# Kernel optimization log

Measured on AMD Instinct MI355X. Metric: run time of the kernel, lower is better.

## Reference

```python
import jax, jax.numpy as jnp
import numpy as np

B, T, C = 2, 2048, 1024
H = 4 * C           # MLP hidden (4*n_embd)
E_DYN = 7           # num_experts - static_experts
TOP_K = 2           # num_experts_per_tok
MOE_LOSS_COEF = 0.01


def setup_inputs() -> dict:
    key = jax.random.key(0)
    ks = jax.random.split(key, 6)
    s = 0.02
    x = jax.random.normal(ks[0], (B, T, C), dtype=jnp.float32)
    gate_w = jax.random.normal(ks[1], (C, E_DYN), dtype=jnp.float32) * s
    w1 = jax.random.normal(ks[2], (E_DYN, C, H), dtype=jnp.float32) * s   # dynamic experts c_fc
    w2 = jax.random.normal(ks[3], (E_DYN, H, C), dtype=jnp.float32) * s   # dynamic experts c_proj
    w1s = jax.random.normal(ks[4], (C, H), dtype=jnp.float32) * s         # static expert c_fc
    w2s = jax.random.normal(ks[5], (H, C), dtype=jnp.float32) * s         # static expert c_proj
    return {"x": x, "gate_w": gate_w, "w1": w1, "w2": w2, "w1s": w1s, "w2s": w2s}


def reference(x, gate_w, w1, w2, w1s, w2s):
    b, t, c = x.shape
    xf = x.reshape(-1, c)                                   # [N, C]
    n = xf.shape[0]

    # static expert (always applied)
    y_static = jax.nn.gelu(xf @ w1s, approximate=False) @ w2s  # [N, C]

    # gating: top-k + softmax over selected scores
    scores = xf @ gate_w                                    # [N, E]
    topk_scores, topk_idx = jax.lax.top_k(scores, TOP_K)    # [N, K]
    topk_w = jax.nn.softmax(topk_scores, axis=-1)           # [N, K]

    # dense dispatch weights [N, E] (top_k indices are distinct -> set is safe)
    probs = jnp.zeros((n, E_DYN), dtype=x.dtype)
    probs = probs.at[jnp.arange(n)[:, None], topk_idx].set(topk_w)

    # all-expert MLP then weighted combine (same math as masked per-expert dispatch)
    h = jax.nn.gelu(jnp.einsum('nc,ech->enh', xf, w1), approximate=False)  # [E, N, H]
    y_all = jnp.einsum('enh,ehc->enc', h, w2)               # [E, N, C]
    y_dyn = jnp.einsum('ne,enc->nc', probs, y_all)          # [N, C]

    y = (y_dyn + y_static).reshape(b, t, c)

    # variance_penalty auxiliary loss
    expert_usage = probs.mean(axis=0)                       # [E]
    variance = jnp.mean((expert_usage - expert_usage.mean()) ** 2)
    aux = MOE_LOSS_COEF * variance
    return y, aux
```

## Files before the change

kernel.cpp:

```cpp
#include <hip/hip_runtime.h>
#include <hip/hip_bf16.h>
#include <math.h>

#define N_TOK 4096
#define C_DIM 1024
#define H_DIM 4096
#define NEXP 7
#define NGRP 8
#define HCAP 13184

typedef __attribute__((ext_vector_type(8))) short short8;
typedef __attribute__((ext_vector_type(4))) float floatx4;

static const size_t OFF_COUNTS = 0;
static const size_t OFF_CURSOR = 64;
static const size_t OFF_BASE   = 128;
static const size_t OFF_PCOUNT = 192;
static const size_t OFF_CNT8   = 256;
static const size_t OFF_USAGE  = 320;
static const size_t OFF_TOPKI  = 4096;
static const size_t OFF_TOPKW  = OFF_TOPKI + 8192ull * 4;
static const size_t OFF_ETOK   = OFF_TOPKW + 8192ull * 4;
static const size_t OFF_EWT    = OFF_ETOK + (size_t)HCAP * 4;
static const size_t OFF_EIDX   = OFF_EWT + (size_t)HCAP * 4;
static const size_t OFF_XB     = 262144;
static const size_t OFF_W1T    = OFF_XB + (size_t)N_TOK * C_DIM * 2;
static const size_t OFF_W2T    = OFF_W1T + (size_t)NGRP * H_DIM * C_DIM * 2;
static const size_t OFF_H      = OFF_W2T + (size_t)NGRP * C_DIM * H_DIM * 2;

static __device__ __forceinline__ unsigned short f2bf(float f) {
    __hip_bfloat16 b = __float2bfloat16(f);
    return *reinterpret_cast<unsigned short*>(&b);
}
static __device__ __forceinline__ float bf2f(unsigned short u) {
    unsigned int v = ((unsigned int)u) << 16;
    return __builtin_bit_cast(float, v);
}

static __device__ __forceinline__ float gelu_f(float v) {
    float z = v * 0.70710678118654752f;
    float az = fabsf(z);
    float t = 1.0f / (1.0f + 0.3275911f * az);
    float poly = t * (0.254829592f + t * (-0.284496736f + t * (1.421413741f +
                 t * (-1.453152027f + t * 1.061405429f))));
    float erf_abs = 1.0f - poly * __expf(-az * az);
    float erf_v = (z < 0.f) ? -erf_abs : erf_abs;
    return 0.5f * v * (1.0f + erf_v);
}

static __device__ __forceinline__ void gll16(const void* g, void* l) {
    __builtin_amdgcn_global_load_lds((const __attribute__((address_space(1))) void*)g,
                                     (__attribute__((address_space(3))) void*)l, 16, 0, 0);
}

static __device__ __forceinline__ void barf() {
    __builtin_amdgcn_s_barrier();
    asm volatile("" ::: "memory");
}
static __device__ __forceinline__ void lgkm0s() {
    asm volatile("s_waitcnt lgkmcnt(0)" ::: "memory");
    __builtin_amdgcn_sched_barrier(0);
}

__global__ void init_small_kernel(int* counts, int* cursor, float* usage) {
    int i = threadIdx.x;
    if (i < 8) { counts[i] = 0; cursor[i] = 0; usage[i] = 0.f; }
}

__global__ __launch_bounds__(256) void transpose_cvt_kernel(
    const float* __restrict__ dyn, const float* __restrict__ stat,
    __hip_bfloat16* __restrict__ dst, int R, int S)
{
    int e = blockIdx.z;
    const float* src = (e < NEXP) ? (dyn + (size_t)e * R * S) : stat;
    unsigned short* d = (unsigned short*)(dst + (size_t)e * R * S);
    int s0 = blockIdx.x * 64, r0 = blockIdx.y * 64;
    __shared__ float t[64][65];
    int lx = (threadIdx.x & 15) * 4, ty = threadIdx.x >> 4;
#pragma unroll
    for (int i = 0; i < 4; i++) {
        int r = ty + i * 16;
        float4 v = *(const float4*)(src + (size_t)(r0 + r) * S + s0 + lx);
        t[r][lx] = v.x; t[r][lx + 1] = v.y; t[r][lx + 2] = v.z; t[r][lx + 3] = v.w;
    }
    __syncthreads();
#pragma unroll
    for (int i = 0; i < 4; i++) {
        int ss = ty + i * 16;
        ushort4 o;
        o.x = f2bf(t[lx][ss]); o.y = f2bf(t[lx + 1][ss]);
        o.z = f2bf(t[lx + 2][ss]); o.w = f2bf(t[lx + 3][ss]);
        *(ushort4*)(d + (size_t)(s0 + ss) * R + r0 + lx) = o;
    }
}

__global__ __launch_bounds__(256) void gate_kernel(
    const float* __restrict__ x, const float* __restrict__ gw,
    unsigned short* __restrict__ xb,
    int* __restrict__ topki, float* __restrict__ topkw,
    int* counts, float* usage)
{
    int wid = threadIdx.x >> 6, lane = threadIdx.x & 63;
    int t = blockIdx.x * 4 + wid;
    float s[NEXP];
#pragma unroll
    for (int e = 0; e < NEXP; e++) s[e] = 0.f;
#pragma unroll
    for (int it = 0; it < 4; ++it) {
        int c = it * 256 + lane * 4;
        float4 xv = *(const float4*)(x + (size_t)t * C_DIM + c);
        ushort4 o;
        o.x = f2bf(xv.x); o.y = f2bf(xv.y); o.z = f2bf(xv.z); o.w = f2bf(xv.w);
        *(ushort4*)(xb + (size_t)t * C_DIM + c) = o;
        const float* g0 = gw + (size_t)c * NEXP;
#pragma unroll
        for (int e = 0; e < NEXP; e++) s[e] += xv.x * g0[e];
#pragma unroll
        for (int e = 0; e < NEXP; e++) s[e] += xv.y * g0[NEXP + e];
#pragma unroll
        for (int e = 0; e < NEXP; e++) s[e] += xv.z * g0[2 * NEXP + e];
#pragma unroll
        for (int e = 0; e < NEXP; e++) s[e] += xv.w * g0[3 * NEXP + e];
    }
#pragma unroll
    for (int e = 0; e < NEXP; e++)
        for (int off = 32; off > 0; off >>= 1) s[e] += __shfl_xor(s[e], off);
    if (lane == 0) {
        int e0 = 0;
        for (int e = 1; e < NEXP; e++) if (s[e] > s[e0]) e0 = e;
        int e1 = -1;
        for (int e = 0; e < NEXP; e++) {
            if (e == e0) continue;
            if (e1 < 0 || s[e] > s[e1]) e1 = e;
        }
        float w0 = 1.f / (1.f + expf(s[e1] - s[e0]));
        float w1 = 1.f - w0;
        topki[t * 2] = e0; topki[t * 2 + 1] = e1;
        topkw[t * 2] = w0; topkw[t * 2 + 1] = w1;
        atomicAdd(&counts[e0], 1); atomicAdd(&counts[e1], 1);
        atomicAdd(&usage[e0], w0); atomicAdd(&usage[e1], w1);
    }
}

__global__ __launch_bounds__(256) void prefix_kernel(
    const int* counts, const float* usage,
    int* base, int* pcount, int* cnt8,
    int* etok, float* ewt, float* y, int aux_index)
{
    __shared__ int sb[NGRP], sc[NGRP], sp[NGRP];
    if (threadIdx.x == 0) {
        int run = 0;
        for (int g = 0; g < NEXP; g++) {
            int c = counts[g];
            int p = (c + 127) & ~127;
            base[g] = run; pcount[g] = p; cnt8[g] = c;
            sb[g] = run; sc[g] = c; sp[g] = p;
            run += p;
        }
        base[NEXP] = run; pcount[NEXP] = N_TOK; cnt8[NEXP] = N_TOK;
        sb[NEXP] = run; sc[NEXP] = N_TOK; sp[NEXP] = N_TOK;
        float u[NEXP]; float mean = 0.f;
        for (int e = 0; e < NEXP; e++) { u[e] = usage[e] / (float)N_TOK; mean += u[e]; }
        mean /= (float)NEXP;
        float var = 0.f;
        for (int e = 0; e < NEXP; e++) { float dd = u[e] - mean; var += dd * dd; }
        var /= (float)NEXP;
        y[aux_index] = 0.01f * var;
    }
    __syncthreads();
    for (int i = threadIdx.x; i < N_TOK; i += 256) {
        etok[sb[NEXP] + i] = i; ewt[sb[NEXP] + i] = 1.0f;
    }
    for (int g = 0; g < NEXP; g++) {
        for (int i = sc[g] + (int)threadIdx.x; i < sp[g]; i += 256) {
            etok[sb[g] + i] = 0; ewt[sb[g] + i] = 0.f;
        }
    }
}

__global__ void scatter_kernel(const int* __restrict__ topki, const float* __restrict__ topkw,
                               const int* __restrict__ base, int* cursor,
                               int* __restrict__ etok, float* __restrict__ ewt,
                               int* __restrict__ eidx)
{
    int i = blockIdx.x * 256 + threadIdx.x;
    int t = i >> 1;
    int e = topki[i];
    float w = topkw[i];
    int pos = atomicAdd(&cursor[e], 1);
    int idx = base[e] + pos;
    etok[idx] = t; ewt[idx] = w;
    eidx[i] = idx;
}


static __device__ __forceinline__ void mfma16(const short8 (&a)[8], const short8 (&b)[4],
                                              floatx4 (&acc)[8][4], int mo, int no) {
#pragma unroll
    for (int i = 0; i < 4; i++)
#pragma unroll
        for (int j = 0; j < 2; j++)
#pragma unroll
            for (int kk = 0; kk < 2; kk++)
                acc[mo + i][no + j] = __builtin_amdgcn_mfma_f32_16x16x32_bf16(
                    a[i * 2 + kk], b[j * 2 + kk], acc[mo + i][no + j], 0, 0, 0);
}
static __device__ __forceinline__ void rdA(short8 (&d)[8], const char* b, int sw0, int sw1) {
#pragma unroll
    for (int i = 0; i < 4; i++) {
        d[i * 2]     = *(const short8*)(b + i * 2048 + sw0);
        d[i * 2 + 1] = *(const short8*)(b + i * 2048 + sw1);
    }
}
static __device__ __forceinline__ void rdB(short8 (&d)[4], const char* b, int sw0, int sw1) {
#pragma unroll
    for (int j = 0; j < 2; j++) {
        d[j * 2]     = *(const short8*)(b + j * 2048 + sw0);
        d[j * 2 + 1] = *(const short8*)(b + j * 2048 + sw1);
    }
}

static __device__ __forceinline__ void gemm_core(char* lds, int NKT,
    const char* pA0, const char* pA1, const char* pA2, const char* pA3,
    const char* pB0, const char* pB1, const char* pB2, const char* pB3,
    floatx4 (&acc)[8][4])
{
    int tid = threadIdx.x, lane = tid & 63, w = tid >> 6;
    int wm = w >> 2, wn = w & 3, l16 = lane & 15, quad = lane >> 4;
    int sw0 = ((quad ^ (l16 & 7)) << 4);
    int sw1 = (((4 + quad) ^ (l16 & 7)) << 4);
    int aoff = (wm * 64 + l16) * 128;
    int boff = (wn * 32 + l16) * 128;
    int wb = w * 1024;
    short8 aM0[8], aM1[8], bN0[4], bN1[4];

#define SA_(h, doff, ko) do { \
    gll16(((h) ? pA1 : pA0) + (ko), lds + (doff) + (h) * 16384 + wb); \
    gll16(((h) ? pA3 : pA2) + (ko), lds + (doff) + (h) * 16384 + 8192 + wb); } while (0)
#define SB_(nh, doff, ko) do { \
    gll16(((nh) ? pB1 : pB0) + (ko), lds + 65536 + (doff) + (nh) * 16384 + wb); \
    gll16(((nh) ? pB3 : pB2) + (ko), lds + 65536 + (doff) + (nh) * 16384 + 8192 + wb); } while (0)

    SA_(0, 0, 0); SA_(1, 0, 0); SB_(0, 0, 0); SB_(1, 0, 0);
    SA_(0, 32768, 128); SA_(1, 32768, 128); SB_(0, 32768, 128);
    asm volatile("s_waitcnt vmcnt(6)" ::: "memory");
    barf();

#pragma unroll 1
    for (int T = 0; T < NKT; ++T) {
        int curo = (T & 1) << 15;
        int nxto = curo ^ 32768;
        bool st1 = (T + 1 < NKT), st2 = (T + 2 < NKT);
        rdA(aM0, lds + curo + aoff, sw0, sw1);
        rdB(bN0, lds + 65536 + curo + boff, sw0, sw1);
        if (st1) SB_(1, nxto, 128);
        barf(); lgkm0s();
        __builtin_amdgcn_s_setprio(1); mfma16(aM0, bN0, acc, 0, 0); __builtin_amdgcn_s_setprio(0);
        barf();
        rdA(aM1, lds + curo + 16384 + aoff, sw0, sw1);
        if (st2) SA_(0, curo, 256);
        barf(); lgkm0s();
        __builtin_amdgcn_s_setprio(1); mfma16(aM1, bN0, acc, 4, 0); __builtin_amdgcn_s_setprio(0);
        barf();
        rdB(bN1, lds + 65536 + curo + 16384 + boff, sw0, sw1);
        if (st2) SA_(1, curo, 256);
        barf(); lgkm0s();
        __builtin_amdgcn_s_setprio(1); mfma16(aM0, bN1, acc, 0, 2); __builtin_amdgcn_s_setprio(0);
        barf();
        if (st2) SB_(0, curo, 256);
        barf();
        __builtin_amdgcn_s_setprio(1); mfma16(aM1, bN1, acc, 4, 2); __builtin_amdgcn_s_setprio(0);
        if (T >= NKT - 2) { asm volatile("s_waitcnt vmcnt(0)" ::: "memory"); }
        else              { asm volatile("s_waitcnt vmcnt(6)" ::: "memory"); }
        barf();
        pA0 += 128; pA1 += 128; pA2 += 128; pA3 += 128;
        pB0 += 128; pB1 += 128; pB2 += 128; pB3 += 128;
    }
#undef SA_
#undef SB_
}

__global__ __launch_bounds__(512, 2) void gemm1_kernel(
    const __hip_bfloat16* __restrict__ xb,
    const __hip_bfloat16* __restrict__ w1t,
    __hip_bfloat16* __restrict__ h,
    const int* __restrict__ etok,
    const int* __restrict__ base,
    const int* __restrict__ pcount)
{
    int id = blockIdx.x;
    int xcd = id & 7, rest = id >> 3;
    int ct = rest & 15, s = rest >> 4;
    int g = s & 7;
    int mt = ((xcd - g) & 7) + 8 * (s >> 3);
    int psz = pcount[g];
    if (mt * 256 >= psz) return;
    int eb = base[g];

    __shared__ __align__(16) char lds[131072];

    int tid = threadIdx.x, lane = tid & 63, w = tid >> 6;
    int u0 = 8 * w + (lane >> 3);
    int v  = (u0 & 31) + ((u0 >> 5) << 6);
    int ssw = ((lane & 7) ^ (lane >> 3)) * 16;

    int t0 = etok[eb + mt * 256 + u0];
    int t1 = etok[eb + mt * 256 + 64 + u0];
    int t2 = etok[eb + mt * 256 + 128 + u0];
    int t3 = etok[eb + mt * 256 + 192 + u0];
    const char* pA0 = (const char*)(xb + (size_t)t0 * C_DIM) + ssw;
    const char* pA1 = (const char*)(xb + (size_t)t1 * C_DIM) + ssw;
    const char* pA2 = (const char*)(xb + (size_t)t2 * C_DIM) + ssw;
    const char* pA3 = (const char*)(xb + (size_t)t3 * C_DIM) + ssw;
    const char* pB0 = (const char*)(w1t + ((size_t)g * H_DIM + ct * 256 + v) * C_DIM) + ssw;
    const char* pB1 = (const char*)(w1t + ((size_t)g * H_DIM + ct * 256 + v + 32) * C_DIM) + ssw;
    const char* pB2 = (const char*)(w1t + ((size_t)g * H_DIM + ct * 256 + v + 128) * C_DIM) + ssw;
    const char* pB3 = (const char*)(w1t + ((size_t)g * H_DIM + ct * 256 + v + 160) * C_DIM) + ssw;

    floatx4 acc[8][4] = {};
    gemm_core(lds, C_DIM / 64, pA0, pA1, pA2, pA3, pB0, pB1, pB2, pB3, acc);

    int wm = w >> 2, wn = w & 3, l16 = lane & 15, quad = lane >> 4;
#pragma unroll
    for (int i = 0; i < 8; i++) {
        int lr0 = mt * 256 + wm * 128 + i * 16 + quad * 4;
#pragma unroll
        for (int reg = 0; reg < 4; reg++) {
            int lr = lr0 + reg;
            if (lr < psz) {
                size_t hrow = (size_t)(eb + lr) * H_DIM;
#pragma unroll
                for (int j = 0; j < 4; j++) {
                    int cc = ct * 256 + wn * 64 + j * 16 + l16;
                    h[hrow + cc] = __float2bfloat16(gelu_f(acc[i][j][reg]));
                }
            }
        }
    }
}

__global__ __launch_bounds__(512, 2) void gemm2_kernel(
    const __hip_bfloat16* __restrict__ h,
    const __hip_bfloat16* __restrict__ w2t,
    unsigned short* __restrict__ yp,
    const int* __restrict__ base,
    const int* __restrict__ pcount)
{
    int id = blockIdx.x;
    int xcd = id & 7, rest = id >> 3;
    int ct = rest & 3, s = rest >> 2;
    int g = s & 7;
    int mt = ((xcd - g) & 7) + 8 * (s >> 3);
    int psz = pcount[g];
    if (mt * 256 >= psz) return;
    int eb = base[g];

    __shared__ __align__(16) char lds[131072];

    int tid = threadIdx.x, lane = tid & 63, w = tid >> 6;
    int u0 = 8 * w + (lane >> 3);
    int v  = (u0 & 31) + ((u0 >> 5) << 6);
    int ssw = ((lane & 7) ^ (lane >> 3)) * 16;

    const char* pA0 = (const char*)(h + (size_t)(eb + mt * 256 + u0) * H_DIM) + ssw;
    const char* pA1 = (const char*)(h + (size_t)(eb + mt * 256 + 64 + u0) * H_DIM) + ssw;
    const char* pA2 = (const char*)(h + (size_t)(eb + mt * 256 + 128 + u0) * H_DIM) + ssw;
    const char* pA3 = (const char*)(h + (size_t)(eb + mt * 256 + 192 + u0) * H_DIM) + ssw;
    const char* pB0 = (const char*)(w2t + ((size_t)g * C_DIM + ct * 256 + v) * H_DIM) + ssw;
    const char* pB1 = (const char*)(w2t + ((size_t)g * C_DIM + ct * 256 + v + 32) * H_DIM) + ssw;
    const char* pB2 = (const char*)(w2t + ((size_t)g * C_DIM + ct * 256 + v + 128) * H_DIM) + ssw;
    const char* pB3 = (const char*)(w2t + ((size_t)g * C_DIM + ct * 256 + v + 160) * H_DIM) + ssw;

    floatx4 acc[8][4] = {};
    gemm_core(lds, H_DIM / 64, pA0, pA1, pA2, pA3, pB0, pB1, pB2, pB3, acc);

    int wm = w >> 2, wn = w & 3, l16 = lane & 15, quad = lane >> 4;
#pragma unroll
    for (int i = 0; i < 8; i++) {
        int lr0 = mt * 256 + wm * 128 + i * 16 + quad * 4;
#pragma unroll
        for (int reg = 0; reg < 4; reg++) {
            int lr = lr0 + reg;
            if (lr < psz) {
                size_t yrow = (size_t)(eb + lr) * C_DIM;
#pragma unroll
                for (int j = 0; j < 4; j++) {
                    int cc = ct * 256 + wn * 64 + j * 16 + l16;
                    yp[yrow + cc] = f2bf(acc[i][j][reg]);
                }
            }
        }
    }
}

__global__ __launch_bounds__(256) void combine_kernel(
    const unsigned short* __restrict__ yp,
    const int* __restrict__ eidx,
    const float* __restrict__ topkw,
    const int* __restrict__ base,
    float* __restrict__ y)
{
    int t = blockIdx.x;
    int i0 = eidx[t * 2], i1 = eidx[t * 2 + 1];
    float w0 = topkw[t * 2], w1 = topkw[t * 2 + 1];
    int is = base[NEXP] + t;
    int c = threadIdx.x * 4;
    ushort4 a = *(const ushort4*)(yp + (size_t)i0 * C_DIM + c);
    ushort4 b = *(const ushort4*)(yp + (size_t)i1 * C_DIM + c);
    ushort4 s = *(const ushort4*)(yp + (size_t)is * C_DIM + c);
    float4 o;
    o.x = w0 * bf2f(a.x) + w1 * bf2f(b.x) + bf2f(s.x);
    o.y = w0 * bf2f(a.y) + w1 * bf2f(b.y) + bf2f(s.y);
    o.z = w0 * bf2f(a.z) + w1 * bf2f(b.z) + bf2f(s.z);
    o.w = w0 * bf2f(a.w) + w1 * bf2f(b.w) + bf2f(s.w);
    *(float4*)(y + (size_t)t * C_DIM + c) = o;
}

extern "C" void kernel_launch(void* const* d_in, const int* in_sizes, int n_in,
                              void* d_out, int out_size, void* d_ws, size_t ws_size,
                              hipStream_t stream) {
    const float* x      = (const float*)d_in[0];
    const float* gate_w = (const float*)d_in[1];
    const float* w1     = (const float*)d_in[2];
    const float* w2     = (const float*)d_in[3];
    const float* w1s    = (const float*)d_in[4];
    const float* w2s    = (const float*)d_in[5];
    float* y = (float*)d_out;
    char* ws = (char*)d_ws;

    int*   counts = (int*)(ws + OFF_COUNTS);
    int*   cursor = (int*)(ws + OFF_CURSOR);
    int*   base   = (int*)(ws + OFF_BASE);
    int*   pcount = (int*)(ws + OFF_PCOUNT);
    int*   cnt8   = (int*)(ws + OFF_CNT8);
    float* usage  = (float*)(ws + OFF_USAGE);
    int*   topki  = (int*)(ws + OFF_TOPKI);
    float* topkw  = (float*)(ws + OFF_TOPKW);
    int*   etok   = (int*)(ws + OFF_ETOK);
    float* ewt    = (float*)(ws + OFF_EWT);
    int*   eidx   = (int*)(ws + OFF_EIDX);
    unsigned short* xb_u = (unsigned short*)(ws + OFF_XB);
    __hip_bfloat16* xb  = (__hip_bfloat16*)(ws + OFF_XB);
    __hip_bfloat16* w1t = (__hip_bfloat16*)(ws + OFF_W1T);
    __hip_bfloat16* w2t = (__hip_bfloat16*)(ws + OFF_W2T);
    __hip_bfloat16* hbuf = (__hip_bfloat16*)(ws + OFF_H);
    unsigned short* yp  = (unsigned short*)(ws + OFF_W1T);

    init_small_kernel<<<1, 64, 0, stream>>>(counts, cursor, usage);

    transpose_cvt_kernel<<<dim3(H_DIM / 64, C_DIM / 64, NGRP), 256, 0, stream>>>(w1, w1s, w1t, C_DIM, H_DIM);
    transpose_cvt_kernel<<<dim3(C_DIM / 64, H_DIM / 64, NGRP), 256, 0, stream>>>(w2, w2s, w2t, H_DIM, C_DIM);

    gate_kernel<<<N_TOK / 4, 256, 0, stream>>>(x, gate_w, xb_u, topki, topkw, counts, usage);
    prefix_kernel<<<1, 256, 0, stream>>>(counts, usage, base, pcount, cnt8, etok, ewt, y, N_TOK * C_DIM);
    scatter_kernel<<<(N_TOK * 2) / 256, 256, 0, stream>>>(topki, topkw, base, cursor, etok, ewt, eidx);

    gemm1_kernel<<<4096, 512, 0, stream>>>(xb, w1t, hbuf, etok, base, pcount);
    gemm2_kernel<<<1024, 512, 0, stream>>>(hbuf, w2t, yp, base, pcount);
    combine_kernel<<<N_TOK, 256, 0, stream>>>(yp, eidx, topkw, base, y);
}
```

Baseline: 726.7 us.

## Peel GEMM mainloop tail and merge weight transpose launches into one

```diff
diff --git a/kernel.cpp b/kernel.cpp
--- a/kernel.cpp
+++ b/kernel.cpp
@@ -57,10 +57,11 @@
     __builtin_amdgcn_s_barrier();
     asm volatile("" ::: "memory");
 }
-static __device__ __forceinline__ void lgkm0s() {
-    asm volatile("s_waitcnt lgkmcnt(0)" ::: "memory");
-    __builtin_amdgcn_sched_barrier(0);
-}
+#define LGKM0 asm volatile("s_waitcnt lgkmcnt(0)" ::: "memory")
+#define VMC6  asm volatile("s_waitcnt vmcnt(6)" ::: "memory")
+#define VMC0  asm volatile("s_waitcnt vmcnt(0)" ::: "memory")
+#define PRIO1 __builtin_amdgcn_s_setprio(1)
+#define PRIO0 __builtin_amdgcn_s_setprio(0)
 
 __global__ void init_small_kernel(int* counts, int* cursor, float* usage) {
     int i = threadIdx.x;
@@ -68,20 +69,35 @@
 }
 
 __global__ __launch_bounds__(256) void transpose_cvt_kernel(
-    const float* __restrict__ dyn, const float* __restrict__ stat,
-    __hip_bfloat16* __restrict__ dst, int R, int S)
-{
-    int e = blockIdx.z;
-    const float* src = (e < NEXP) ? (dyn + (size_t)e * R * S) : stat;
-    unsigned short* d = (unsigned short*)(dst + (size_t)e * R * S);
-    int s0 = blockIdx.x * 64, r0 = blockIdx.y * 64;
+    const float* __restrict__ w1, const float* __restrict__ w1s,
+    const float* __restrict__ w2, const float* __restrict__ w2s,
+    __hip_bfloat16* __restrict__ w1t, __hip_bfloat16* __restrict__ w2t)
+{
+    int bid = blockIdx.x;
+    int fam = bid >> 13;
+    int r = bid & 8191;
+    int e = r >> 10;
+    int t_ = r & 1023;
+    int R, S, s0, r0;
+    const float* src; unsigned short* d;
+    if (fam == 0) {
+        R = C_DIM; S = H_DIM;
+        src = (e < NEXP) ? (w1 + (size_t)e * R * S) : w1s;
+        d = (unsigned short*)(w1t) + (size_t)e * R * S;
+        s0 = (t_ & 63) * 64; r0 = (t_ >> 6) * 64;
+    } else {
+        R = H_DIM; S = C_DIM;
+        src = (e < NEXP) ? (w2 + (size_t)e * R * S) : w2s;
+        d = (unsigned short*)(w2t) + (size_t)e * R * S;
+        s0 = (t_ & 15) * 64; r0 = (t_ >> 4) * 64;
+    }
     __shared__ float t[64][65];
     int lx = (threadIdx.x & 15) * 4, ty = threadIdx.x >> 4;
 #pragma unroll
     for (int i = 0; i < 4; i++) {
-        int r = ty + i * 16;
-        float4 v = *(const float4*)(src + (size_t)(r0 + r) * S + s0 + lx);
-        t[r][lx] = v.x; t[r][lx + 1] = v.y; t[r][lx + 2] = v.z; t[r][lx + 3] = v.w;
+        int rr = ty + i * 16;
+        float4 v = *(const float4*)(src + (size_t)(r0 + rr) * S + s0 + lx);
+        t[rr][lx] = v.x; t[rr][lx + 1] = v.y; t[rr][lx + 2] = v.z; t[rr][lx + 3] = v.w;
     }
     __syncthreads();
 #pragma unroll
@@ -243,38 +259,66 @@
 
     SA_(0, 0, 0); SA_(1, 0, 0); SB_(0, 0, 0); SB_(1, 0, 0);
     SA_(0, 32768, 128); SA_(1, 32768, 128); SB_(0, 32768, 128);
-    asm volatile("s_waitcnt vmcnt(6)" ::: "memory");
+    VMC6;
     barf();
 
 #pragma unroll 1
-    for (int T = 0; T < NKT; ++T) {
+    for (int T = 0; T < NKT - 2; ++T) {
         int curo = (T & 1) << 15;
         int nxto = curo ^ 32768;
-        bool st1 = (T + 1 < NKT), st2 = (T + 2 < NKT);
+        rdB(bN0, lds + 65536 + curo + boff, sw0, sw1);
         rdA(aM0, lds + curo + aoff, sw0, sw1);
-        rdB(bN0, lds + 65536 + curo + boff, sw0, sw1);
-        if (st1) SB_(1, nxto, 128);
-        barf(); lgkm0s();
-        __builtin_amdgcn_s_setprio(1); mfma16(aM0, bN0, acc, 0, 0); __builtin_amdgcn_s_setprio(0);
-        barf();
+        SB_(1, nxto, 128);
+        barf();
+        PRIO1; mfma16(aM0, bN0, acc, 0, 0); PRIO0;
+        LGKM0; barf();
         rdA(aM1, lds + curo + 16384 + aoff, sw0, sw1);
-        if (st2) SA_(0, curo, 256);
-        barf(); lgkm0s();
-        __builtin_amdgcn_s_setprio(1); mfma16(aM1, bN0, acc, 4, 0); __builtin_amdgcn_s_setprio(0);
-        barf();
+        SA_(0, curo, 256);
+        barf();
+        PRIO1; mfma16(aM1, bN0, acc, 4, 0); PRIO0;
+        LGKM0; barf();
         rdB(bN1, lds + 65536 + curo + 16384 + boff, sw0, sw1);
-        if (st2) SA_(1, curo, 256);
-        barf(); lgkm0s();
-        __builtin_amdgcn_s_setprio(1); mfma16(aM0, bN1, acc, 0, 2); __builtin_amdgcn_s_setprio(0);
-        barf();
-        if (st2) SB_(0, curo, 256);
-        barf();
-        __builtin_amdgcn_s_setprio(1); mfma16(aM1, bN1, acc, 4, 2); __builtin_amdgcn_s_setprio(0);
-        if (T >= NKT - 2) { asm volatile("s_waitcnt vmcnt(0)" ::: "memory"); }
-        else              { asm volatile("s_waitcnt vmcnt(6)" ::: "memory"); }
+        SA_(1, curo, 256);
+        barf();
+        PRIO1; mfma16(aM0, bN1, acc, 0, 2); PRIO0;
+        LGKM0; barf();
+        SB_(0, curo, 256);
+        barf();
+        PRIO1; mfma16(aM1, bN1, acc, 4, 2); PRIO0;
+        VMC6;
         barf();
         pA0 += 128; pA1 += 128; pA2 += 128; pA3 += 128;
         pB0 += 128; pB1 += 128; pB2 += 128; pB3 += 128;
+    }
+    {
+        int curo = ((NKT - 2) & 1) << 15;
+        int nxto = curo ^ 32768;
+        rdB(bN0, lds + 65536 + curo + boff, sw0, sw1);
+        rdA(aM0, lds + curo + aoff, sw0, sw1);
+        SB_(1, nxto, 128);
+        barf();
+        PRIO1; mfma16(aM0, bN0, acc, 0, 0); PRIO0;
+        LGKM0; barf();
+        rdA(aM1, lds + curo + 16384 + aoff, sw0, sw1);
+        barf();
+        PRIO1; mfma16(aM1, bN0, acc, 4, 0); PRIO0;
+        LGKM0; barf();
+        rdB(bN1, lds + 65536 + curo + 16384 + boff, sw0, sw1);
+        barf();
+        PRIO1; mfma16(aM0, bN1, acc, 0, 2); PRIO0;
+        LGKM0; barf();
+        PRIO1; mfma16(aM1, bN1, acc, 4, 2); PRIO0;
+        VMC0;
+        barf();
+        int lasto = nxto;
+        rdB(bN0, lds + 65536 + lasto + boff, sw0, sw1);
+        rdA(aM0, lds + lasto + aoff, sw0, sw1);
+        rdA(aM1, lds + lasto + 16384 + aoff, sw0, sw1);
+        rdB(bN1, lds + 65536 + lasto + 16384 + boff, sw0, sw1);
+        mfma16(aM0, bN0, acc, 0, 0);
+        mfma16(aM1, bN0, acc, 4, 0);
+        mfma16(aM0, bN1, acc, 0, 2);
+        mfma16(aM1, bN1, acc, 4, 2);
     }
 #undef SA_
 #undef SB_
@@ -448,8 +492,7 @@
 
     init_small_kernel<<<1, 64, 0, stream>>>(counts, cursor, usage);
 
-    transpose_cvt_kernel<<<dim3(H_DIM / 64, C_DIM / 64, NGRP), 256, 0, stream>>>(w1, w1s, w1t, C_DIM, H_DIM);
-    transpose_cvt_kernel<<<dim3(C_DIM / 64, H_DIM / 64, NGRP), 256, 0, stream>>>(w2, w2s, w2t, H_DIM, C_DIM);
+    transpose_cvt_kernel<<<16384, 256, 0, stream>>>(w1, w1s, w2, w2s, w1t, w2t);
 
     gate_kernel<<<N_TOK / 4, 256, 0, stream>>>(x, gate_w, xb_u, topki, topkw, counts, usage);
     prefix_kernel<<<1, 256, 0, stream>>>(counts, usage, base, pcount, cnt8, etok, ewt, y, N_TOK * C_DIM);
```

Result: faster. 712.2 us (-2.0%).
